# Kernel optimization log

Measured on AMD Instinct MI355X. Metric: run time of the kernel, lower is better.

Reference implementation:

```python
import jax, jax.numpy as jnp
import numpy as np

B = 1024
N_CPGS = 20000
N_FREQS = N_CPGS // 2 + 1  # 10001
HIDDEN = (256, 128, 64)
LN_EPS = 1e-5


def setup_inputs() -> dict:
    key = jax.random.key(0)
    keys = jax.random.split(key, 16)
    inp = {"x": jax.random.normal(keys[0], (B, N_CPGS), dtype=jnp.float32)}
    in_dim = N_FREQS
    for i, h in enumerate(HIDDEN):
        inp[f"W{i}"] = jax.random.normal(keys[1 + i], (h, in_dim), dtype=jnp.float32) * 0.01
        inp[f"alpha{i}"] = jnp.full((h, in_dim), 0.01, dtype=jnp.float32)
        inp[f"b{i}"] = jnp.zeros((h,), dtype=jnp.float32)
        inp[f"eta{i}"] = jnp.asarray(0.1, dtype=jnp.float32)
        inp[f"g{i}"] = jnp.ones((h,), dtype=jnp.float32)   # LayerNorm gamma
        inp[f"be{i}"] = jnp.zeros((h,), dtype=jnp.float32)  # LayerNorm beta
        in_dim = h
    inp["head_w"] = jax.random.normal(keys[10], (1, in_dim), dtype=jnp.float32) * (1.0 / np.sqrt(in_dim))
    inp["head_b"] = jnp.zeros((1,), dtype=jnp.float32)
    return inp


def _hebbian_layer(x, W, alpha, b, eta):
    # y_slow = x W^T + b;  plastic[b,i] = eta * tanh(y_slow)[b,i] * sum_j sigmoid(alpha)[i,j] * x_norm[b,j] * x[b,j]
    y_slow = jnp.einsum('bd,hd->bh', x, W) + b
    x_norm = x / (jnp.linalg.norm(x, axis=-1, keepdims=True) + 1e-8)
    c = x_norm * x  # (B, in) -- collapses the (B,out,in) outer-product trace algebraically
    plastic = eta * jnp.tanh(y_slow) * jnp.einsum('bd,hd->bh', c, jax.nn.sigmoid(alpha))
    return y_slow + plastic


def _layer_norm(h, g, be):
    mu = jnp.mean(h, axis=-1, keepdims=True)
    var = jnp.mean((h - mu) ** 2, axis=-1, keepdims=True)
    return (h - mu) * jax.lax.rsqrt(var + LN_EPS) * g + be


def reference(x, W0, alpha0, b0, eta0, g0, be0,
              W1, alpha1, b1, eta1, g1, be1,
              W2, alpha2, b2, eta2, g2, be2,
              head_w, head_b):
    # FFT spectral front-end
    xc = x - jnp.mean(x, axis=1, keepdims=True)
    h = jnp.log1p(jnp.abs(jnp.fft.rfft(xc, axis=1)))  # (B, N_FREQS)
    params = [(W0, alpha0, b0, eta0, g0, be0),
              (W1, alpha1, b1, eta1, g1, be1),
              (W2, alpha2, b2, eta2, g2, be2)]
    for (W, a, b, eta, g, be) in params:
        h = jax.nn.gelu(_layer_norm(_hebbian_layer(h, W, a, b, eta), g, be), approximate=False)
        # dropout is identity in eval mode
    return (jnp.einsum('bd,od->bo', h, head_w) + head_b)[:, 0]  # (B,)
```

## Files before the change

kernel.cpp:

```cpp
#include <hip/hip_runtime.h>
#include <hip/hip_bf16.h>
#include <math.h>

typedef short bf16x8 __attribute__((ext_vector_type(8)));
typedef float f32x4 __attribute__((ext_vector_type(4)));

static __device__ __forceinline__ unsigned short f2bf(float f) {
    unsigned int u = __float_as_uint(f);
    unsigned int r = (u + 0x7fffu + ((u >> 16) & 1u)) >> 16;
    return (unsigned short)r;
}

static __device__ __forceinline__ float gelu_f(float x) {
    return 0.5f * x * (1.f + erff(x * 0.70710678118654752f));
}

static __device__ __forceinline__ void gload_lds16(const void* g, void* l) {
    __builtin_amdgcn_global_load_lds(
        (const __attribute__((address_space(1))) unsigned int*)g,
        (__attribute__((address_space(3))) unsigned int*)l, 16, 0, 0);
}

static __device__ __forceinline__ int ldsmap(int i) { return i + (i >> 6); }

static __device__ __forceinline__ int rev4(int k) {
    int d0 = k % 10; k /= 10;
    int d1 = k % 10; k /= 10;
    int d2 = k % 10; int d3 = k / 10;
    return d0 * 1000 + d1 * 100 + d2 * 10 + d3;
}

static __device__ __forceinline__ void dft5(
    float a0r, float a0i, float a1r, float a1i, float a2r, float a2i,
    float a3r, float a3i, float a4r, float a4i,
    float* Xr, float* Xi)
{
    const float c1 = 0.30901699437494742f, c2 = -0.80901699437494745f;
    const float s1 = 0.95105651629515357f, s2 = 0.58778525229247312f;
    float t1r = a1r + a4r, t1i = a1i + a4i;
    float d1r = a1r - a4r, d1i = a1i - a4i;
    float t2r = a2r + a3r, t2i = a2i + a3i;
    float d2r = a2r - a3r, d2i = a2i - a3i;
    Xr[0] = a0r + t1r + t2r; Xi[0] = a0i + t1i + t2i;
    float m1r = a0r + c1 * t1r + c2 * t2r, m1i = a0i + c1 * t1i + c2 * t2i;
    float m2r = a0r + c2 * t1r + c1 * t2r, m2i = a0i + c2 * t1i + c1 * t2i;
    float n1r = s1 * d1r + s2 * d2r, n1i = s1 * d1i + s2 * d2i;
    float n2r = s2 * d1r - s1 * d2r, n2i = s2 * d1i - s1 * d2i;
    Xr[1] = m1r + n1i; Xi[1] = m1i - n1r;
    Xr[4] = m1r - n1i; Xi[4] = m1i + n1r;
    Xr[2] = m2r + n2i; Xi[2] = m2i - n2r;
    Xr[3] = m2r - n2i; Xi[3] = m2i + n2r;
}

template<int S>
static __device__ __forceinline__ void radix10_stage(
    float* __restrict__ reb, float* __restrict__ imb, int tid, float mean)
{
    constexpr int L  = (S == 0) ? 1000 : (S == 1) ? 100 : (S == 2) ? 10 : 1;
    constexpr int SC = (S == 0) ? 1 : (S == 1) ? 10 : (S == 2) ? 100 : 1000;
    constexpr bool TW = (S != 3);

    const float WR[5] = {1.f, 0.80901699437494745f, 0.30901699437494742f,
                         -0.30901699437494742f, -0.80901699437494745f};
    const float WI[5] = {0.f, -0.58778525229247312f, -0.95105651629515357f,
                         -0.95105651629515357f, -0.58778525229247312f};

    for (int w = tid; w < 1000; w += 512) {
        int g, j;
        if (S == 0)      { g = 0; j = w; }
        else if (S == 3) { g = w; j = 0; }
        else             { g = w / L; j = w - g * L; }
        const int base = g * (10 * L) + j;

        float ar[10], ai[10];
        #pragma unroll
        for (int u = 0; u < 10; ++u) {
            int idx = ldsmap(base + u * L);
            ar[u] = reb[idx];
            ai[u] = imb[idx];
        }
        if (S == 0) {
            #pragma unroll
            for (int u = 0; u < 10; ++u) { ar[u] -= mean; ai[u] -= mean; }
        }

        float Er[5], Ei[5], Or[5], Oi[5];
        dft5(ar[0], ai[0], ar[2], ai[2], ar[4], ai[4], ar[6], ai[6], ar[8], ai[8], Er, Ei);
        dft5(ar[1], ai[1], ar[3], ai[3], ar[5], ai[5], ar[7], ai[7], ar[9], ai[9], Or, Oi);
        #pragma unroll
        for (int k = 1; k < 5; ++k) {
            float tr = Or[k] * WR[k] - Oi[k] * WI[k];
            Oi[k] = Or[k] * WI[k] + Oi[k] * WR[k];
            Or[k] = tr;
        }

        if (TW) {
            const float ang = (float)(j * SC) * -6.28318530717958648e-4f;
            float w1c, w1s;
            __sincosf(ang, &w1s, &w1c);
            float twr[10], twi[10];
            twr[0] = 1.f; twi[0] = 0.f;
            #pragma unroll
            for (int t = 1; t < 10; ++t) {
                twr[t] = twr[t - 1] * w1c - twi[t - 1] * w1s;
                twi[t] = twr[t - 1] * w1s + twi[t - 1] * w1c;
            }
            #pragma unroll
            for (int k = 0; k < 5; ++k) {
                float xr0 = Er[k] + Or[k], xi0 = Ei[k] + Oi[k];
                float xr1 = Er[k] - Or[k], xi1 = Ei[k] - Oi[k];
                int i0 = ldsmap(base + k * L);
                int i1 = ldsmap(base + (k + 5) * L);
                if (k == 0) {
                    reb[i0] = xr0;
                    imb[i0] = xi0;
                } else {
                    reb[i0] = xr0 * twr[k] - xi0 * twi[k];
                    imb[i0] = xr0 * twi[k] + xi0 * twr[k];
                }
                reb[i1] = xr1 * twr[k + 5] - xi1 * twi[k + 5];
                imb[i1] = xr1 * twi[k + 5] + xi1 * twr[k + 5];
            }
        } else {
            #pragma unroll
            for (int k = 0; k < 5; ++k) {
                int i0 = ldsmap(base + k * L);
                int i1 = ldsmap(base + (k + 5) * L);
                reb[i0] = Er[k] + Or[k]; imb[i0] = Ei[k] + Oi[k];
                reb[i1] = Er[k] - Or[k]; imb[i1] = Ei[k] - Oi[k];
            }
        }
    }
}

__global__ __launch_bounds__(512, 4)
void fft_prep_kernel(const float* __restrict__ x,
                     unsigned short* __restrict__ hb,
                     unsigned short* __restrict__ cb,
                     const float* __restrict__ W0, const float* __restrict__ A0,
                     unsigned short* __restrict__ Wb, unsigned short* __restrict__ Sb,
                     const float* __restrict__ W1, const float* __restrict__ A1,
                     const float* __restrict__ W2, const float* __restrict__ A2,
                     float* __restrict__ W1T, float* __restrict__ S1T,
                     float* __restrict__ W2T, float* __restrict__ S2T)
{
    if (blockIdx.x >= 1024) {
        int idx = (blockIdx.x - 1024) * 512 + threadIdx.x;
        if (idx < 1280128) {
            const bool isW = idx < 640064;
            const int f4 = isW ? idx : idx - 640064;
            const float* src = isW ? W0 : A0;
            unsigned short* dst = isW ? Wb : Sb;
            float4 v = ((const float4*)src)[f4];
            float e[4] = {v.x, v.y, v.z, v.w};
            int flat = f4 * 4;
            int row = flat / 10001;
            int col = flat - row * 10001;
            #pragma unroll
            for (int i = 0; i < 4; ++i) {
                if (col == 10001) { row++; col = 0; }
                float val = isW ? e[i] : 1.f / (1.f + expf(-e[i]));
                dst[(size_t)row * 10240 + col] = f2bf(val);
                col++;
            }
        } else if (idx < 1341312) {
            int i = idx - 1280128;
            int row = i / 239;
            int col = 10001 + (i - row * 239);
            Wb[(size_t)row * 10240 + col] = 0;
            Sb[(size_t)row * 10240 + col] = 0;
        } else if (idx < 1423232) {
            int o = idx - 1341312;
            if (o < 32768) {
                int d = o >> 7, h = o & 127;
                W1T[o] = W1[h * 256 + d];
            } else if (o < 65536) {
                int p = o - 32768;
                int d = p >> 7, h = p & 127;
                S1T[p] = 1.f / (1.f + expf(-A1[h * 256 + d]));
            } else if (o < 73728) {
                int p = o - 65536;
                int d = p >> 6, h = p & 63;
                W2T[p] = W2[h * 128 + d];
            } else {
                int p = o - 73728;
                int d = p >> 6, h = p & 63;
                S2T[p] = 1.f / (1.f + expf(-A2[h * 128 + d]));
            }
        }
        return;
    }

    __shared__ float reb[10156];
    __shared__ float imb[10156];
    __shared__ float redbuf[8];

    const int b = blockIdx.x;
    const int tid = threadIdx.x;
    const int lane = tid & 63;
    const int wv = tid >> 6;
    const float* xr = x + (size_t)b * 20000;

    float sum = 0.f;
    for (int i4 = tid; i4 < 5000; i4 += 512) {
        float4 v = ((const float4*)xr)[i4];
        sum += v.x + v.y + v.z + v.w;
        int n = i4 * 2;
        reb[ldsmap(n)]     = v.x; imb[ldsmap(n)]     = v.y;
        reb[ldsmap(n + 1)] = v.z; imb[ldsmap(n + 1)] = v.w;
    }
    #pragma unroll
    for (int o = 32; o; o >>= 1) sum += __shfl_xor(sum, o);
    __syncthreads();
    if (lane == 0) redbuf[wv] = sum;
    __syncthreads();
    float tot = 0.f;
    #pragma unroll
    for (int i = 0; i < 8; ++i) tot += redbuf[i];
    const float mean = tot * (1.f / 20000.f);

    radix10_stage<0>(reb, imb, tid, mean);
    __syncthreads();
    radix10_stage<1>(reb, imb, tid, 0.f);
    __syncthreads();
    radix10_stage<2>(reb, imb, tid, 0.f);
    __syncthreads();
    radix10_stage<3>(reb, imb, tid, 0.f);
    __syncthreads();

    float harr[20];
    float sumsq = 0.f;
    unsigned short* hrow = hb + (size_t)b * 10240;
    #pragma unroll
    for (int i = 0; i < 20; ++i) {
        int k = tid + i * 512;
        float hval = 0.f;
        if (k <= 10000) {
            int k1 = (k == 10000) ? 0 : k;
            int k2 = (10000 - k) % 10000;
            int i1 = ldsmap(rev4(k1));
            int i2 = ldsmap(rev4(k2));
            float zr = reb[i1], zi = imb[i1];
            float wr = reb[i2], wi = imb[i2];
            float er = 0.5f * (zr + wr);
            float ei = 0.5f * (zi - wi);
            float odr = 0.5f * (zi + wi);
            float odi = -0.5f * (zr - wr);
            float ct, st;
            __sincosf((float)k * -3.14159265358979324e-4f, &st, &ct);
            float xre = er + ct * odr - st * odi;
            float xim = ei + ct * odi + st * odr;
            hval = log1pf(sqrtf(xre * xre + xim * xim));
        }
        harr[i] = hval;
        hrow[k] = f2bf(hval);
        sumsq += hval * hval;
    }
    #pragma unroll
    for (int o = 32; o; o >>= 1) sumsq += __shfl_xor(sumsq, o);
    __syncthreads();
    if (lane == 0) redbuf[wv] = sumsq;
    __syncthreads();
    float tsq = 0.f;
    #pragma unroll
    for (int i = 0; i < 8; ++i) tsq += redbuf[i];
    const float inv = 1.f / (sqrtf(tsq) + 1e-8f);

    unsigned short* crow = cb + (size_t)b * 10240;
    #pragma unroll
    for (int i = 0; i < 20; ++i) {
        int k = tid + i * 512;
        crow[k] = f2bf(harr[i] * harr[i] * inv);
    }
}

__global__ __launch_bounds__(256, 2)
void gemm0_kernel(const unsigned short* __restrict__ hb, const unsigned short* __restrict__ cb,
                  const unsigned short* __restrict__ Wb, const unsigned short* __restrict__ Sb,
                  float* __restrict__ Py, float* __restrict__ Pp)
{
    __shared__ unsigned short Ah[128 * 64];
    __shared__ unsigned short Ac[128 * 64];
    __shared__ unsigned short Bw[64 * 64];
    __shared__ unsigned short Bs[64 * 64];

    const int t = threadIdx.x;
    const int b0 = blockIdx.x * 128;
    const int n0 = blockIdx.y * 64;
    const int z = blockIdx.z;
    const int lane = t & 63;
    const int wv = t >> 6;
    const int ml = lane & 15;
    const int q4 = lane >> 4;
    const int s0 = q4 ^ (ml & 7);

    const int sub = lane >> 3;
    const int sl = lane & 7;
    const int gsw = sl ^ sub;

    f32x4 accY[2][4], accP[2][4];
    #pragma unroll
    for (int mt = 0; mt < 2; ++mt)
        #pragma unroll
        for (int nt = 0; nt < 4; ++nt) {
            accY[mt][nt] = (f32x4){0.f, 0.f, 0.f, 0.f};
            accP[mt][nt] = (f32x4){0.f, 0.f, 0.f, 0.f};
        }

    const int kbase = z * 640;

    for (int step = 0; step < 10; ++step) {
        const int k0 = kbase + step * 64;
        __syncthreads();
        #pragma unroll
        for (int j = 0; j < 4; ++j) {
            const int c = wv * 4 + j;
            const size_t go = (size_t)(b0 + c * 8 + sub) * 10240 + k0 + gsw * 8;
            gload_lds16(&hb[go], &Ah[c * 512]);
            gload_lds16(&cb[go], &Ac[c * 512]);
        }
        #pragma unroll
        for (int j = 0; j < 2; ++j) {
            const int c = wv * 2 + j;
            const size_t go = (size_t)(n0 + c * 8 + sub) * 10240 + k0 + gsw * 8;
            gload_lds16(&Wb[go], &Bw[c * 512]);
            gload_lds16(&Sb[go], &Bs[c * 512]);
        }
        __syncthreads();

        #pragma unroll
        for (int kk = 0; kk < 2; ++kk) {
            const int slot = (s0 ^ (kk << 2)) << 3;
            bf16x8 ah[2], ac[2], bw[4], bs[4];
            #pragma unroll
            for (int mt = 0; mt < 2; ++mt) {
                int mrow = wv * 32 + mt * 16 + ml;
                ah[mt] = *(const bf16x8*)&Ah[mrow * 64 + slot];
                ac[mt] = *(const bf16x8*)&Ac[mrow * 64 + slot];
            }
            #pragma unroll
            for (int nt = 0; nt < 4; ++nt) {
                int nrow = nt * 16 + ml;
                bw[nt] = *(const bf16x8*)&Bw[nrow * 64 + slot];
                bs[nt] = *(const bf16x8*)&Bs[nrow * 64 + slot];
            }
            #pragma unroll
            for (int mt = 0; mt < 2; ++mt)
                #pragma unroll
                for (int nt = 0; nt < 4; ++nt) {
                    accY[mt][nt] = __builtin_amdgcn_mfma_f32_16x16x32_bf16(ah[mt], bw[nt], accY[mt][nt], 0, 0, 0);
                    accP[mt][nt] = __builtin_amdgcn_mfma_f32_16x16x32_bf16(ac[mt], bs[nt], accP[mt][nt], 0, 0, 0);
                }
        }
    }

    const int rq = q4 * 4;
    #pragma unroll
    for (int mt = 0; mt < 2; ++mt)
        #pragma unroll
        for (int nt = 0; nt < 4; ++nt)
            #pragma unroll
            for (int r = 0; r < 4; ++r) {
                int m = b0 + wv * 32 + mt * 16 + rq + r;
                int n = n0 + nt * 16 + ml;
                size_t o = ((size_t)z * 1024 + m) * 256 + n;
                Py[o] = accY[mt][nt][r];
                Pp[o] = accP[mt][nt][r];
            }
}

__global__ __launch_bounds__(256)
void combine0_kernel(const float* __restrict__ Py, const float* __restrict__ Pp,
                     const float* __restrict__ b0v, const float* __restrict__ eta0p,
                     const float* __restrict__ g0, const float* __restrict__ be0,
                     float* __restrict__ h1, float* __restrict__ c1)
{
    __shared__ float red[4];
    const int b = blockIdx.x;
    const int h = threadIdx.x;
    const int lane = h & 63;
    const int wv = h >> 6;

    float ys = 0.f, ps = 0.f;
    for (int s = 0; s < 16; ++s) {
        size_t o = ((size_t)s * 1024 + b) * 256 + h;
        ys += Py[o];
        ps += Pp[o];
    }
    float y = ys + b0v[h];
    float v = y + eta0p[0] * tanhf(y) * ps;

    float s1 = v;
    #pragma unroll
    for (int o = 32; o; o >>= 1) s1 += __shfl_xor(s1, o);
    __syncthreads();
    if (lane == 0) red[wv] = s1;
    __syncthreads();
    float sum = red[0] + red[1] + red[2] + red[3];

    float s2 = v * v;
    #pragma unroll
    for (int o = 32; o; o >>= 1) s2 += __shfl_xor(s2, o);
    __syncthreads();
    if (lane == 0) red[wv] = s2;
    __syncthreads();
    float sumsq = red[0] + red[1] + red[2] + red[3];

    float mu = sum * (1.f / 256.f);
    float var = sumsq * (1.f / 256.f) - mu * mu;
    float u = (v - mu) * rsqrtf(var + 1e-5f) * g0[h] + be0[h];
    float gl = gelu_f(u);

    float s3 = gl * gl;
    #pragma unroll
    for (int o = 32; o; o >>= 1) s3 += __shfl_xor(s3, o);
    __syncthreads();
    if (lane == 0) red[wv] = s3;
    __syncthreads();
    float gsq = red[0] + red[1] + red[2] + red[3];
    float inv = 1.f / (sqrtf(gsq) + 1e-8f);

    h1[(size_t)b * 256 + h] = gl;
    c1[(size_t)b * 256 + h] = gl * gl * inv;
}

__global__ __launch_bounds__(256)
void tail_kernel(const float* __restrict__ h1, const float* __restrict__ c1,
                 const float* __restrict__ W1T, const float* __restrict__ S1T,
                 const float* __restrict__ b1, const float* __restrict__ eta1p,
                 const float* __restrict__ g1, const float* __restrict__ be1,
                 const float* __restrict__ W2T, const float* __restrict__ S2T,
                 const float* __restrict__ b2, const float* __restrict__ eta2p,
                 const float* __restrict__ g2, const float* __restrict__ be2,
                 const float* __restrict__ hw, const float* __restrict__ hbod,
                 float* __restrict__ out)
{
    __shared__ float sh[4][256];
    __shared__ float sc[4][256];
    __shared__ float sv[4][128];
    __shared__ float sh2[4][128];
    __shared__ float sc2[4][128];
    __shared__ float sv2[4][64];

    const int t = threadIdx.x;
    const int b0 = blockIdx.x * 4;
    const int lane = t & 63;
    const int wv = t >> 6;

    #pragma unroll
    for (int i = 0; i < 4; ++i) {
        int idx = t + i * 256;
        int r = idx >> 8, d = idx & 255;
        sh[r][d] = h1[(size_t)(b0 + r) * 256 + d];
        sc[r][d] = c1[(size_t)(b0 + r) * 256 + d];
    }
    __syncthreads();

    const int hcol = t & 127;
    const int r2 = t >> 7;
    float ya[2] = {0.f, 0.f};
    float pa[2] = {0.f, 0.f};
    for (int d = 0; d < 256; ++d) {
        float w = W1T[d * 128 + hcol];
        float s = S1T[d * 128 + hcol];
        #pragma unroll
        for (int i = 0; i < 2; ++i) {
            int r = r2 * 2 + i;
            ya[i] += sh[r][d] * w;
            pa[i] += sc[r][d] * s;
        }
    }
    const float e1 = eta1p[0];
    #pragma unroll
    for (int i = 0; i < 2; ++i) {
        int r = r2 * 2 + i;
        float y = ya[i] + b1[hcol];
        sv[r][hcol] = y + e1 * tanhf(y) * pa[i];
    }
    __syncthreads();

    {
        int r = wv;
        float v0 = sv[r][lane];
        float v1 = sv[r][lane + 64];
        float s = v0 + v1, sq = v0 * v0 + v1 * v1;
        #pragma unroll
        for (int o = 32; o; o >>= 1) { s += __shfl_xor(s, o); sq += __shfl_xor(sq, o); }
        float mu = s * (1.f / 128.f);
        float var = sq * (1.f / 128.f) - mu * mu;
        float rs = rsqrtf(var + 1e-5f);
        float u0 = (v0 - mu) * rs * g1[lane] + be1[lane];
        float u1 = (v1 - mu) * rs * g1[lane + 64] + be1[lane + 64];
        float ge0 = gelu_f(u0);
        float ge1 = gelu_f(u1);
        float gsq = ge0 * ge0 + ge1 * ge1;
        #pragma unroll
        for (int o = 32; o; o >>= 1) gsq += __shfl_xor(gsq, o);
        float inv = 1.f / (sqrtf(gsq) + 1e-8f);
        sh2[r][lane] = ge0; sh2[r][lane + 64] = ge1;
        sc2[r][lane] = ge0 * ge0 * inv; sc2[r][lane + 64] = ge1 * ge1 * inv;
    }
    __syncthreads();

    const int h2c = t & 63;
    const int r4 = t >> 6;
    float yb = 0.f, pb = 0.f;
    for (int d = 0; d < 128; ++d) {
        yb += sh2[r4][d] * W2T[d * 64 + h2c];
        pb += sc2[r4][d] * S2T[d * 64 + h2c];
    }
    {
        const float e2 = eta2p[0];
        float y = yb + b2[h2c];
        sv2[r4][h2c] = y + e2 * tanhf(y) * pb;
    }
    __syncthreads();

    {
        int r = wv;
        float v0 = sv2[r][lane];
        float s = v0, sq = v0 * v0;
        #pragma unroll
        for (int o = 32; o; o >>= 1) { s += __shfl_xor(s, o); sq += __shfl_xor(sq, o); }
        float mu = s * (1.f / 64.f);
        float var = sq * (1.f / 64.f) - mu * mu;
        float rs = rsqrtf(var + 1e-5f);
        float u = (v0 - mu) * rs * g2[lane] + be2[lane];
        float g = gelu_f(u);
        float hc = g * hw[lane];
        #pragma unroll
        for (int o = 32; o; o >>= 1) hc += __shfl_xor(hc, o);
        if (lane == 0) out[b0 + r] = hc + hbod[0];
    }
}

extern "C" void kernel_launch(void* const* d_in, const int* in_sizes, int n_in,
                              void* d_out, int out_size, void* d_ws, size_t ws_size,
                              hipStream_t stream)
{
    const float* x    = (const float*)d_in[0];
    const float* W0   = (const float*)d_in[1];
    const float* A0   = (const float*)d_in[2];
    const float* b0   = (const float*)d_in[3];
    const float* eta0 = (const float*)d_in[4];
    const float* g0   = (const float*)d_in[5];
    const float* be0  = (const float*)d_in[6];
    const float* W1   = (const float*)d_in[7];
    const float* A1   = (const float*)d_in[8];
    const float* b1   = (const float*)d_in[9];
    const float* eta1 = (const float*)d_in[10];
    const float* g1   = (const float*)d_in[11];
    const float* be1  = (const float*)d_in[12];
    const float* W2   = (const float*)d_in[13];
    const float* A2   = (const float*)d_in[14];
    const float* b2   = (const float*)d_in[15];
    const float* eta2 = (const float*)d_in[16];
    const float* g2   = (const float*)d_in[17];
    const float* be2  = (const float*)d_in[18];
    const float* hw   = (const float*)d_in[19];
    const float* hbod = (const float*)d_in[20];
    float* out = (float*)d_out;

    char* w = (char*)d_ws;
    unsigned short* hb  = (unsigned short*)(w + 0);
    unsigned short* cb  = (unsigned short*)(w + 20971520);
    unsigned short* Wb0 = (unsigned short*)(w + 41943040);
    unsigned short* Sb0 = (unsigned short*)(w + 47185920);
    float* Py  = (float*)(w + 52428800);
    float* Pp  = (float*)(w + 69206016);
    float* h1  = (float*)(w + 85983232);
    float* c1  = (float*)(w + 87031808);
    float* W1T = (float*)(w + 88080384);
    float* S1T = (float*)(w + 88211456);
    float* W2T = (float*)(w + 88342528);
    float* S2T = (float*)(w + 88375296);

    hipLaunchKernelGGL(fft_prep_kernel, dim3(3804), dim3(512), 0, stream,
                       x, hb, cb, W0, A0, Wb0, Sb0, W1, A1, W2, A2, W1T, S1T, W2T, S2T);
    hipLaunchKernelGGL(gemm0_kernel, dim3(8, 4, 16), dim3(256), 0, stream, hb, cb, Wb0, Sb0, Py, Pp);
    hipLaunchKernelGGL(combine0_kernel, dim3(1024), dim3(256), 0, stream, Py, Pp, b0, eta0, g0, be0, h1, c1);
    hipLaunchKernelGGL(tail_kernel, dim3(256), dim3(256), 0, stream, h1, c1, W1T, S1T, b1, eta1, g1, be1,
                       W2T, S2T, b2, eta2, g2, be2, hw, hbod, out);
}
```

Measured before the change: 281.9 us.

## Compute squared activations in GEMM and apply per-row norm after reduction

Instead of writing a second bf16 matrix c = h*h/||h|| from the FFT kernel, the FFT kernel now stores only a per-row inverse norm. The GEMM squares the bf16 h fragments in registers to form the plastic-path operand, and the combine kernel multiplies by the row norm afterwards. This removes a 20 MB write, its later read and one LDS tile per step. The cost is extra VALU conversion work inside the MFMA loop and a slightly different rounding, since h is rounded to bf16 before squaring.

```diff
diff --git a/kernel.cpp b/kernel.cpp
--- a/kernel.cpp
+++ b/kernel.cpp
@@ -9,6 +9,18 @@
     unsigned int u = __float_as_uint(f);
     unsigned int r = (u + 0x7fffu + ((u >> 16) & 1u)) >> 16;
     return (unsigned short)r;
+}
+
+static __device__ __forceinline__ bf16x8 sq_bf16x8(bf16x8 a) {
+    bf16x8 r;
+    #pragma unroll
+    for (int i = 0; i < 8; ++i) {
+        unsigned int u = ((unsigned int)(unsigned short)a[i]) << 16;
+        float f = __uint_as_float(u);
+        f *= f;
+        r[i] = (short)f2bf(f);
+    }
+    return r;
 }
 
 static __device__ __forceinline__ float gelu_f(float x) {
@@ -136,7 +148,7 @@
 __global__ __launch_bounds__(512, 4)
 void fft_prep_kernel(const float* __restrict__ x,
                      unsigned short* __restrict__ hb,
-                     unsigned short* __restrict__ cb,
+                     float* __restrict__ hnorm,
                      const float* __restrict__ W0, const float* __restrict__ A0,
                      unsigned short* __restrict__ Wb, unsigned short* __restrict__ Sb,
                      const float* __restrict__ W1, const float* __restrict__ A1,
@@ -228,7 +240,6 @@
     radix10_stage<3>(reb, imb, tid, 0.f);
     __syncthreads();
 
-    float harr[20];
     float sumsq = 0.f;
     unsigned short* hrow = hb + (size_t)b * 10240;
     #pragma unroll
@@ -252,7 +263,6 @@
             float xim = ei + ct * odi + st * odr;
             hval = log1pf(sqrtf(xre * xre + xim * xim));
         }
-        harr[i] = hval;
         hrow[k] = f2bf(hval);
         sumsq += hval * hval;
     }
@@ -261,26 +271,20 @@
     __syncthreads();
     if (lane == 0) redbuf[wv] = sumsq;
     __syncthreads();
-    float tsq = 0.f;
-    #pragma unroll
-    for (int i = 0; i < 8; ++i) tsq += redbuf[i];
-    const float inv = 1.f / (sqrtf(tsq) + 1e-8f);
-
-    unsigned short* crow = cb + (size_t)b * 10240;
-    #pragma unroll
-    for (int i = 0; i < 20; ++i) {
-        int k = tid + i * 512;
-        crow[k] = f2bf(harr[i] * harr[i] * inv);
+    if (tid == 0) {
+        float tsq = 0.f;
+        #pragma unroll
+        for (int i = 0; i < 8; ++i) tsq += redbuf[i];
+        hnorm[b] = 1.f / (sqrtf(tsq) + 1e-8f);
     }
 }
 
 __global__ __launch_bounds__(256, 2)
-void gemm0_kernel(const unsigned short* __restrict__ hb, const unsigned short* __restrict__ cb,
+void gemm0_kernel(const unsigned short* __restrict__ hb,
                   const unsigned short* __restrict__ Wb, const unsigned short* __restrict__ Sb,
                   float* __restrict__ Py, float* __restrict__ Pp)
 {
     __shared__ unsigned short Ah[128 * 64];
-    __shared__ unsigned short Ac[128 * 64];
     __shared__ unsigned short Bw[64 * 64];
     __shared__ unsigned short Bs[64 * 64];
 
@@ -317,7 +321,6 @@
             const int c = wv * 4 + j;
             const size_t go = (size_t)(b0 + c * 8 + sub) * 10240 + k0 + gsw * 8;
             gload_lds16(&hb[go], &Ah[c * 512]);
-            gload_lds16(&cb[go], &Ac[c * 512]);
         }
         #pragma unroll
         for (int j = 0; j < 2; ++j) {
@@ -336,7 +339,7 @@
             for (int mt = 0; mt < 2; ++mt) {
                 int mrow = wv * 32 + mt * 16 + ml;
                 ah[mt] = *(const bf16x8*)&Ah[mrow * 64 + slot];
-                ac[mt] = *(const bf16x8*)&Ac[mrow * 64 + slot];
+                ac[mt] = sq_bf16x8(ah[mt]);
             }
             #pragma unroll
             for (int nt = 0; nt < 4; ++nt) {
@@ -371,6 +374,7 @@
 
 __global__ __launch_bounds__(256)
 void combine0_kernel(const float* __restrict__ Py, const float* __restrict__ Pp,
+                     const float* __restrict__ hnorm,
                      const float* __restrict__ b0v, const float* __restrict__ eta0p,
                      const float* __restrict__ g0, const float* __restrict__ be0,
                      float* __restrict__ h1, float* __restrict__ c1)
@@ -387,6 +391,7 @@
         ys += Py[o];
         ps += Pp[o];
     }
+    ps *= hnorm[b];
     float y = ys + b0v[h];
     float v = y + eta0p[0] * tanhf(y) * ps;
 
@@ -563,22 +568,22 @@
 
     char* w = (char*)d_ws;
     unsigned short* hb  = (unsigned short*)(w + 0);
-    unsigned short* cb  = (unsigned short*)(w + 20971520);
-    unsigned short* Wb0 = (unsigned short*)(w + 41943040);
-    unsigned short* Sb0 = (unsigned short*)(w + 47185920);
-    float* Py  = (float*)(w + 52428800);
-    float* Pp  = (float*)(w + 69206016);
-    float* h1  = (float*)(w + 85983232);
-    float* c1  = (float*)(w + 87031808);
-    float* W1T = (float*)(w + 88080384);
-    float* S1T = (float*)(w + 88211456);
-    float* W2T = (float*)(w + 88342528);
-    float* S2T = (float*)(w + 88375296);
+    unsigned short* Wb0 = (unsigned short*)(w + 20971520);
+    unsigned short* Sb0 = (unsigned short*)(w + 26214400);
+    float* Py   = (float*)(w + 31457280);
+    float* Pp   = (float*)(w + 48234496);
+    float* h1   = (float*)(w + 65011712);
+    float* c1   = (float*)(w + 66060288);
+    float* W1T  = (float*)(w + 67108864);
+    float* S1T  = (float*)(w + 67239936);
+    float* W2T  = (float*)(w + 67371008);
+    float* S2T  = (float*)(w + 67403776);
+    float* hnm  = (float*)(w + 67436544);
 
     hipLaunchKernelGGL(fft_prep_kernel, dim3(3804), dim3(512), 0, stream,
-                       x, hb, cb, W0, A0, Wb0, Sb0, W1, A1, W2, A2, W1T, S1T, W2T, S2T);
-    hipLaunchKernelGGL(gemm0_kernel, dim3(8, 4, 16), dim3(256), 0, stream, hb, cb, Wb0, Sb0, Py, Pp);
-    hipLaunchKernelGGL(combine0_kernel, dim3(1024), dim3(256), 0, stream, Py, Pp, b0, eta0, g0, be0, h1, c1);
+                       x, hb, hnm, W0, A0, Wb0, Sb0, W1, A1, W2, A2, W1T, S1T, W2T, S2T);
+    hipLaunchKernelGGL(gemm0_kernel, dim3(8, 4, 16), dim3(256), 0, stream, hb, Wb0, Sb0, Py, Pp);
+    hipLaunchKernelGGL(combine0_kernel, dim3(1024), dim3(256), 0, stream, Py, Pp, hnm, b0, eta0, g0, be0, h1, c1);
     hipLaunchKernelGGL(tail_kernel, dim3(256), dim3(256), 0, stream, h1, c1, W1T, S1T, b1, eta1, g1, be1,
                        W2T, S2T, b2, eta2, g2, be2, hw, hbod, out);
 }
```

Result: no change. 282.2 us (+0.1%).
